# Kernel tuning notes

Measured on AMD Instinct MI355X. Metric: run time of the kernel, lower is better.

## Reference

```python
import jax, jax.numpy as jnp
import numpy as np

B, N, IN_DIM, HID, OUT_DIM, CODEBOOK = 32, 2048, 128, 64, 64, 2048


def setup_inputs() -> dict:
    key = jax.random.key(0)
    ks = jax.random.split(key, 6)
    # xavier-uniform-ish scales for the MLP weights
    def xavier(k, fan_in, fan_out):
        gain = float(np.sqrt(2.0))  # relu gain
        lim = gain * np.sqrt(6.0 / (fan_in + fan_out))
        return jax.random.uniform(k, (fan_in, fan_out), jnp.float32, -lim, lim)
    return {
        "obs": jax.random.normal(ks[0], (B, N, IN_DIM), jnp.float32),
        "W1": xavier(ks[1], IN_DIM, HID),
        "b1": jnp.full((HID,), 0.01, jnp.float32),
        "W2": xavier(ks[2], HID, HID),
        "b2": jnp.full((HID,), 0.01, jnp.float32),
        "W3": xavier(ks[3], HID, OUT_DIM),
        "b3": jnp.full((OUT_DIM,), 0.01, jnp.float32),
        "codebook": jax.random.normal(ks[4], (CODEBOOK, OUT_DIM), jnp.float32),
    }


def reference(obs, W1, b1, W2, b2, W3, b3, codebook):
    # --- tiny MLP ---
    h = jax.nn.relu(obs @ W1 + b1)
    h = jax.nn.relu(h @ W2 + b2)
    x = h @ W3 + b3  # [B, N, D]

    # --- vector quantize: euclidean nearest codebook entry ---
    x2 = jnp.sum(x * x, axis=-1, keepdims=True)           # [B, N, 1]
    e2 = jnp.sum(codebook * codebook, axis=-1)            # [C]
    dist = x2 - 2.0 * jnp.einsum("bnd,cd->bnc", x, codebook) + e2  # [B, N, C]
    idx = jnp.argmin(dist, axis=-1)                        # [B, N] int
    quantize = codebook[idx]                               # [B, N, D] gather

    # commitment loss: mse(sg(quantize), x)
    cmt_loss = jnp.mean((jax.lax.stop_gradient(quantize) - x) ** 2)
    # straight-through estimator
    msg = x + jax.lax.stop_gradient(quantize - x)
    return (msg, idx, cmt_loss)
```

## Files before the change

kernel.cpp:

```cpp
#include <hip/hip_runtime.h>


#define NPTS    65536
#define IN_DIM  128
#define HID     64
#define OUT_DIM 64
#define CB_N    2048
#define MSG_ELEMS (NPTS * OUT_DIM)
#define LOSS_SCALE (1.0f / 4194304.0f)
#define MARG 0.5f
#define CAND_CAP 1024
#define BPTS 128
#define NTHR 512

typedef __attribute__((ext_vector_type(8))) short short8;
typedef _Float16 half8 __attribute__((ext_vector_type(8)));
typedef __attribute__((ext_vector_type(4))) float f32x4;
typedef unsigned int u32;
typedef unsigned long long u64;

__device__ __forceinline__ void gld16(void* lds_base, const void* gsrc) {
    __builtin_amdgcn_global_load_lds(
        (const __attribute__((address_space(1))) u32*)gsrc,
        (__attribute__((address_space(3))) u32*)lds_base, 16, 0, 0);
}

__global__ __launch_bounds__(256) void prep_all(
    const float* __restrict__ cb,
    const float* __restrict__ W1, const float* __restrict__ W2,
    const float* __restrict__ W3,
    float* __restrict__ e2,
    _Float16* __restrict__ cbh,
    _Float16* __restrict__ w1h, _Float16* __restrict__ w1l,
    _Float16* __restrict__ w2h, _Float16* __restrict__ w2l,
    _Float16* __restrict__ w3h, _Float16* __restrict__ w3l,
    float* __restrict__ loss)
{
    const int b = blockIdx.x, tid = threadIdx.x;
    if (b < 64) {
        const int id = b * 256 + tid;
        const int n = id >> 3, h = (id >> 2) & 1, quad = id & 3;
        const int t = n >> 4, l15 = n & 15;
        const float* src = cb + (long)n * OUT_DIM + h * 32 + quad * 8;
        half8 hi;
        #pragma unroll
        for (int j = 0; j < 8; ++j)
            hi[j] = (_Float16)src[j];
        const long dst = ((long)(t * 2 + h) * 64 + quad * 16 + l15) * 8;
        *(half8*)(cbh + dst) = hi;
    } else if (b < 72) {
        const int id = (b - 64) * 256 + tid;
        const int lane = id & 63;
        const int m = lane & 15, quad = lane >> 4;
        const float* W; _Float16 *dh, *dl; int frag;
        if (id < 1024)      { W = W1; dh = w1h; dl = w1l; frag = id >> 6; }
        else if (id < 1536) { W = W2; dh = w2h; dl = w2l; frag = (id - 1024) >> 6; }
        else                { W = W3; dh = w3h; dl = w3l; frag = (id - 1536) >> 6; }
        const int kc = frag >> 2, nt = frag & 3;
        half8 hi, lo;
        #pragma unroll
        for (int j = 0; j < 8; ++j) {
            const float v = W[(long)(kc * 32 + quad * 8 + j) * 64 + nt * 16 + m];
            hi[j] = (_Float16)v;
            lo[j] = (_Float16)(v - (float)hi[j]);
        }
        const long dst = (long)(frag * 64 + lane) * 8;
        *(half8*)(dh + dst) = hi;
        *(half8*)(dl + dst) = lo;
    } else {
        if (b == 72 && tid == 0) *loss = 0.0f;
        const int c = (b - 72) * 256 + tid;
        const float4* row = (const float4*)(cb + (long)c * OUT_DIM);
        float s = 0.0f;
        #pragma unroll
        for (int mq = 0; mq < 16; ++mq) {
            const float4 v = row[mq];
            s += v.x * v.x + v.y * v.y + v.z * v.z + v.w * v.w;
        }
        e2[c] = s;
    }
}

#define MFMA16(A, B, C) __builtin_amdgcn_mfma_f32_16x16x32_f16(A, B, C, 0, 0, 0)

__device__ __forceinline__ void split16(const float* xs, half8& h, half8& l) {
    #pragma unroll
    for (int j = 0; j < 8; ++j) {
        h[j] = (_Float16)xs[j];
        l[j] = (_Float16)(xs[j] - (float)h[j]);
    }
}

__device__ __forceinline__ u64 packkey(float d, int n) {
    u32 ub = __float_as_uint(d);
    ub = (ub & 0x80000000u) ? ~ub : (ub | 0x80000000u);
    return ((u64)ub << 32) | (u32)n;
}

__device__ __forceinline__ float exdist(
    const float* xr, const float* __restrict__ cbrow, float e2v)
{
    const float4* xp = (const float4*)xr;
    const float4* cp = (const float4*)cbrow;
    float a0 = 0.0f, a1 = 0.0f;
    #pragma unroll
    for (int mq = 0; mq < 16; ++mq) {
        const float4 xv = xp[mq], cv = cp[mq];
        a0 = fmaf(xv.x, cv.x, a0); a1 = fmaf(xv.y, cv.y, a1);
        a0 = fmaf(xv.z, cv.z, a0); a1 = fmaf(xv.w, cv.w, a1);
    }
    return fmaf(-2.0f, a0 + a1, e2v);
}

__global__ __launch_bounds__(NTHR, 4) void fused_mlp_vq(
    const float* __restrict__ obs,
    const float* __restrict__ b1, const float* __restrict__ b2,
    const float* __restrict__ b3,
    const _Float16* __restrict__ w1h, const _Float16* __restrict__ w1l,
    const _Float16* __restrict__ w2h, const _Float16* __restrict__ w2l,
    const _Float16* __restrict__ w3h, const _Float16* __restrict__ w3l,
    const float* __restrict__ cb,
    const _Float16* __restrict__ cbhp,
    const float* __restrict__ e2,
    float* __restrict__ msg,
    float* __restrict__ idx_out,
    float* __restrict__ loss_out)
{
    __shared__ float hbuf[BPTS * 68];
    __shared__ __align__(16) char stg[2][16384];
    __shared__ int   cand_pc[CAND_CAP];
    __shared__ u64   keys[BPTS];
    __shared__ int   win_sh[BPTS];
    __shared__ int   idx_sh[BPTS];
    __shared__ float wred[NTHR / 64];
    __shared__ int   cand_cnt;

    const int t = threadIdx.x, lane = t & 63, w = t >> 6;
    const int m = lane & 15, quad = lane >> 4;
    const long base = (long)blockIdx.x * BPTS;
    const int row0 = w * 16 + quad * 4;
    const int arow_l = w * 16 + m;

    if (t == 0) cand_cnt = 0;
    if (t < BPTS) keys[t] = ~0ULL;

    {
        float bb1[4], bb2[4], bb3[4];
        #pragma unroll
        for (int nt = 0; nt < 4; ++nt) {
            bb1[nt] = b1[nt * 16 + m];
            bb2[nt] = b2[nt * 16 + m];
            bb3[nt] = b3[nt * 16 + m];
        }

        const float* arow = obs + (base + w * 16 + m) * IN_DIM;
        half8 a1h[4], a1l[4];
        #pragma unroll
        for (int kc = 0; kc < 4; ++kc) {
            const float4 va = *(const float4*)(arow + kc * 32 + quad * 8);
            const float4 vb = *(const float4*)(arow + kc * 32 + quad * 8 + 4);
            const float xs[8] = {va.x, va.y, va.z, va.w, vb.x, vb.y, vb.z, vb.w};
            split16(xs, a1h[kc], a1l[kc]);
        }

        #pragma unroll
        for (int nt = 0; nt < 4; ++nt) {
            f32x4 acc = {0.0f, 0.0f, 0.0f, 0.0f};
            #pragma unroll
            for (int kc = 0; kc < 4; ++kc) {
                const long fo = (long)((kc * 4 + nt) * 64 + lane) * 8;
                const half8 wh = *(const half8*)(w1h + fo);
                const half8 wl = *(const half8*)(w1l + fo);
                acc = MFMA16(a1h[kc], wh, acc);
                acc = MFMA16(a1l[kc], wh, acc);
                acc = MFMA16(a1h[kc], wl, acc);
            }
            #pragma unroll
            for (int r = 0; r < 4; ++r) {
                const float v = acc[r] + bb1[nt];
                hbuf[(row0 + r) * 68 + nt * 16 + m] = v > 0.0f ? v : 0.0f;
            }
        }

        half8 a2h[2], a2l[2];
        #pragma unroll
        for (int kc = 0; kc < 2; ++kc) {
            const float4 va = *(const float4*)&hbuf[arow_l * 68 + kc * 32 + quad * 8];
            const float4 vb = *(const float4*)&hbuf[arow_l * 68 + kc * 32 + quad * 8 + 4];
            const float xs[8] = {va.x, va.y, va.z, va.w, vb.x, vb.y, vb.z, vb.w};
            split16(xs, a2h[kc], a2l[kc]);
        }
        #pragma unroll
        for (int nt = 0; nt < 4; ++nt) {
            f32x4 acc = {0.0f, 0.0f, 0.0f, 0.0f};
            #pragma unroll
            for (int kc = 0; kc < 2; ++kc) {
                const long fo = (long)((kc * 4 + nt) * 64 + lane) * 8;
                const half8 wh = *(const half8*)(w2h + fo);
                const half8 wl = *(const half8*)(w2l + fo);
                acc = MFMA16(a2h[kc], wh, acc);
                acc = MFMA16(a2l[kc], wh, acc);
                acc = MFMA16(a2h[kc], wl, acc);
            }
            #pragma unroll
            for (int r = 0; r < 4; ++r) {
                const float v = acc[r] + bb2[nt];
                hbuf[(row0 + r) * 68 + nt * 16 + m] = v > 0.0f ? v : 0.0f;
            }
        }

        half8 a3h[2], a3l[2];
        #pragma unroll
        for (int kc = 0; kc < 2; ++kc) {
            const float4 va = *(const float4*)&hbuf[arow_l * 68 + kc * 32 + quad * 8];
            const float4 vb = *(const float4*)&hbuf[arow_l * 68 + kc * 32 + quad * 8 + 4];
            const float xs[8] = {va.x, va.y, va.z, va.w, vb.x, vb.y, vb.z, vb.w};
            split16(xs, a3h[kc], a3l[kc]);
        }
        #pragma unroll
        for (int nt = 0; nt < 4; ++nt) {
            f32x4 acc = {0.0f, 0.0f, 0.0f, 0.0f};
            #pragma unroll
            for (int kc = 0; kc < 2; ++kc) {
                const long fo = (long)((kc * 4 + nt) * 64 + lane) * 8;
                const half8 wh = *(const half8*)(w3h + fo);
                const half8 wl = *(const half8*)(w3l + fo);
                acc = MFMA16(a3h[kc], wh, acc);
                acc = MFMA16(a3l[kc], wh, acc);
                acc = MFMA16(a3h[kc], wl, acc);
            }
            #pragma unroll
            for (int r = 0; r < 4; ++r)
                hbuf[(row0 + r) * 68 + nt * 16 + m] = acc[r] + bb3[nt];
        }
    }

    half8 a0h, a1h;
    {
        const float* xrow = &hbuf[(w * 16 + m) * 68];
        const float4 xa = *(const float4*)(xrow + quad * 8);
        const float4 xb = *(const float4*)(xrow + quad * 8 + 4);
        const float4 xc = *(const float4*)(xrow + 32 + quad * 8);
        const float4 xd = *(const float4*)(xrow + 32 + quad * 8 + 4);
        const float x0[8] = {xa.x, xa.y, xa.z, xa.w, xb.x, xb.y, xb.z, xb.w};
        const float x1[8] = {xc.x, xc.y, xc.z, xc.w, xd.x, xd.y, xd.z, xd.w};
        #pragma unroll
        for (int j = 0; j < 8; ++j) {
            a0h[j] = (_Float16)x0[j];
            a1h[j] = (_Float16)x1[j];
        }
    }

    #pragma unroll
    for (int j = 0; j < 2; ++j)
        gld16(stg[0] + (w * 2 + j) * 1024,
              cbhp + (w * 2 + j) * 512 + lane * 8);
    __syncthreads();

    float bd[4] = {3.4e38f, 3.4e38f, 3.4e38f, 3.4e38f};
    int   bi[4] = {0, 0, 0, 0};

    for (int ph = 0; ph < 16; ++ph) {
        if (ph < 15) {
            const _Float16* cbq = cbhp + (long)(ph + 1) * 8192;
            #pragma unroll
            for (int j = 0; j < 2; ++j)
                gld16(stg[(ph + 1) & 1] + (w * 2 + j) * 1024,
                      cbq + (w * 2 + j) * 512 + lane * 8);
        }
        const char* bufp = stg[ph & 1];

        half8 th[16];
        float e2v[8];
        #pragma unroll
        for (int tl = 0; tl < 8; ++tl) {
            th[tl * 2]     = *(const half8*)(bufp + tl * 2048 + lane * 16);
            th[tl * 2 + 1] = *(const half8*)(bufp + tl * 2048 + 1024 + lane * 16);
            e2v[tl] = e2[(ph * 8 + tl) * 16 + m];
        }

        f32x4 acc[8];
        __builtin_amdgcn_s_setprio(1);
        #pragma unroll
        for (int tl = 0; tl < 8; ++tl) {
            f32x4 z = {0.0f, 0.0f, 0.0f, 0.0f};
            z = MFMA16(a0h, th[tl * 2], z);
            z = MFMA16(a1h, th[tl * 2 + 1], z);
            acc[tl] = z;
        }
        __builtin_amdgcn_s_setprio(0);

        #pragma unroll
        for (int tl = 0; tl < 8; ++tl) {
            const int g = ph * 8 + tl;
            const int code = g * 16 + m;
            bool pushm[4]; int pip[4];
            #pragma unroll
            for (int r = 0; r < 4; ++r) {
                const float d = fmaf(-2.0f, acc[tl][r], e2v[tl]);
                const bool lt = d < bd[r];
                pushm[r] = __builtin_fabsf(d - bd[r]) < MARG;
                pip[r] = lt ? bi[r] : code;
                bd[r] = lt ? d : bd[r];
                bi[r] = lt ? code : bi[r];
            }
            if (__any((int)(pushm[0] | pushm[1] | pushm[2] | pushm[3]))) {
                #pragma unroll
                for (int r = 0; r < 4; ++r) {
                    if (pushm[r]) {
                        const int slot = atomicAdd(&cand_cnt, 1);
                        if (slot < CAND_CAP)
                            cand_pc[slot] = ((w * 16 + quad * 4 + r) << 16) | pip[r];
                    }
                }
            }
        }
        __syncthreads();
    }

    {
        float rd[4]; int ri[4];
        #pragma unroll
        for (int r = 0; r < 4; ++r) { rd[r] = bd[r]; ri[r] = bi[r]; }
        #pragma unroll
        for (int off = 1; off <= 8; off <<= 1) {
            #pragma unroll
            for (int r = 0; r < 4; ++r) {
                const float od = __shfl_xor(rd[r], off, 64);
                const int   oi = __shfl_xor(ri[r], off, 64);
                if (od < rd[r] || (od == rd[r] && oi < ri[r])) {
                    rd[r] = od; ri[r] = oi;
                }
            }
        }
        #pragma unroll
        for (int r = 0; r < 4; ++r) {
            const int pl = w * 16 + quad * 4 + r;
            if (m == 0) win_sh[pl] = ri[r];
            if (bd[r] <= rd[r] + MARG && bi[r] != ri[r]) {
                const int slot = atomicAdd(&cand_cnt, 1);
                if (slot < CAND_CAP)
                    cand_pc[slot] = (pl << 16) | bi[r];
            }
        }
    }
    __syncthreads();

    {
        if (t < BPTS) {
            const int n = win_sh[t];
            const float ex = exdist(&hbuf[t * 68], cb + (long)n * OUT_DIM, e2[n]);
            atomicMin(&keys[t], packkey(ex, n));
        }
        const int L = min(cand_cnt, CAND_CAP);
        for (int l = t; l < L; l += NTHR) {
            const int pc = cand_pc[l];
            const int p = pc >> 16, n = pc & 0xFFFF;
            const float ex = exdist(&hbuf[p * 68], cb + (long)n * OUT_DIM, e2[n]);
            atomicMin(&keys[p], packkey(ex, n));
        }
    }
    __syncthreads();

    if (t < BPTS) {
        const int code = (int)(keys[t] & 0xFFFFFFFFu);
        idx_sh[t] = code;
        idx_out[base + t] = (float)code;
    }
    __syncthreads();

    float lsum = 0.0f;
    float4* mg = (float4*)(msg + base * OUT_DIM);
    #pragma unroll
    for (int mm = 0; mm < 4; ++mm) {
        const int v = t + NTHR * mm;
        const int p = v >> 4, k4 = v & 15;
        const int code = idx_sh[p];
        const float4 q = ((const float4*)(cb + (long)code * OUT_DIM))[k4];
        const float4 xv = *(const float4*)&hbuf[p * 68 + k4 * 4];
        const float dx = q.x - xv.x, dy = q.y - xv.y;
        const float dz = q.z - xv.z, dw2 = q.w - xv.w;
        lsum += dx * dx + dy * dy + dz * dz + dw2 * dw2;
        mg[v] = q;
    }
    #pragma unroll
    for (int off = 32; off > 0; off >>= 1) lsum += __shfl_down(lsum, off, 64);
    if (lane == 0) wred[w] = lsum;
    __syncthreads();
    if (t == 0) {
        float s = 0.0f;
        #pragma unroll
        for (int i = 0; i < NTHR / 64; ++i) s += wred[i];
        atomicAdd(loss_out, s * LOSS_SCALE);
    }
}

extern "C" void kernel_launch(void* const* d_in, const int* in_sizes, int n_in,
                              void* d_out, int out_size, void* d_ws, size_t ws_size,
                              hipStream_t stream) {
    const float* obs = (const float*)d_in[0];
    const float* W1  = (const float*)d_in[1];
    const float* b1  = (const float*)d_in[2];
    const float* W2  = (const float*)d_in[3];
    const float* b2  = (const float*)d_in[4];
    const float* W3  = (const float*)d_in[5];
    const float* b3  = (const float*)d_in[6];
    const float* cb  = (const float*)d_in[7];

    float* out  = (float*)d_out;
    float* msg  = out;
    float* idxf = out + MSG_ELEMS;
    float* loss = out + MSG_ELEMS + NPTS;

    char* ws = (char*)d_ws;
    float*     e2  = (float*)ws;
    _Float16*  cbh = (_Float16*)(ws + 8192);
    _Float16* w1h = (_Float16*)(ws + 532480);
    _Float16* w1l = (_Float16*)(ws + 548864);
    _Float16* w2h = (_Float16*)(ws + 565248);
    _Float16* w2l = (_Float16*)(ws + 573440);
    _Float16* w3h = (_Float16*)(ws + 581632);
    _Float16* w3l = (_Float16*)(ws + 589824);

    prep_all<<<80, 256, 0, stream>>>(cb, W1, W2, W3, e2, cbh,
                                     w1h, w1l, w2h, w2l, w3h, w3l, loss);
    fused_mlp_vq<<<NPTS / BPTS, NTHR, 0, stream>>>(
        obs, b1, b2, b3, w1h, w1l, w2h, w2l, w3h, w3l,
        cb, cbh, e2, msg, idxf, loss);
}
```

Before: 157.0 us.

## Stagger codebook phase order per block and aggregate candidate atomics per wave

Each block now starts its walk over the 16 codebook chunks at an offset derived from its block index, so concurrent blocks read different parts of the codebook instead of the same lines at once. Candidate pushes into the shared list now use one ballot-based atomicAdd per wave with mbcnt prefix offsets, replacing one LDS atomic per pushing lane. The point is to spread L2 traffic and cut contention on the shared counter. It adds some ballot and popcount work on the push path, and the changed visiting order can change tie-breaking in the running argmin.

```diff
diff --git a/kernel.cpp b/kernel.cpp
--- a/kernel.cpp
+++ b/kernel.cpp
@@ -140,6 +140,7 @@
     const long base = (long)blockIdx.x * BPTS;
     const int row0 = w * 16 + quad * 4;
     const int arow_l = w * 16 + m;
+    const int ofs = blockIdx.x & 15;
 
     if (t == 0) cand_cnt = 0;
     if (t < BPTS) keys[t] = ~0ULL;
@@ -254,15 +255,17 @@
     #pragma unroll
     for (int j = 0; j < 2; ++j)
         gld16(stg[0] + (w * 2 + j) * 1024,
-              cbhp + (w * 2 + j) * 512 + lane * 8);
+              cbhp + (long)ofs * 8192 + (w * 2 + j) * 512 + lane * 8);
     __syncthreads();
 
     float bd[4] = {3.4e38f, 3.4e38f, 3.4e38f, 3.4e38f};
     int   bi[4] = {0, 0, 0, 0};
 
     for (int ph = 0; ph < 16; ++ph) {
+        const int pp = (ph + ofs) & 15;
         if (ph < 15) {
-            const _Float16* cbq = cbhp + (long)(ph + 1) * 8192;
+            const int pn = (ph + 1 + ofs) & 15;
+            const _Float16* cbq = cbhp + (long)pn * 8192;
             #pragma unroll
             for (int j = 0; j < 2; ++j)
                 gld16(stg[(ph + 1) & 1] + (w * 2 + j) * 1024,
@@ -276,7 +279,7 @@
         for (int tl = 0; tl < 8; ++tl) {
             th[tl * 2]     = *(const half8*)(bufp + tl * 2048 + lane * 16);
             th[tl * 2 + 1] = *(const half8*)(bufp + tl * 2048 + 1024 + lane * 16);
-            e2v[tl] = e2[(ph * 8 + tl) * 16 + m];
+            e2v[tl] = e2[(pp * 8 + tl) * 16 + m];
         }
 
         f32x4 acc[8];
@@ -292,7 +295,7 @@
 
         #pragma unroll
         for (int tl = 0; tl < 8; ++tl) {
-            const int g = ph * 8 + tl;
+            const int g = pp * 8 + tl;
             const int code = g * 16 + m;
             bool pushm[4]; int pip[4];
             #pragma unroll
@@ -305,13 +308,30 @@
                 bi[r] = lt ? code : bi[r];
             }
             if (__any((int)(pushm[0] | pushm[1] | pushm[2] | pushm[3]))) {
+                u64 mk[4]; int cnt[4];
+                int tot = 0;
+                #pragma unroll
+                for (int r = 0; r < 4; ++r) {
+                    mk[r] = __ballot((int)pushm[r]);
+                    cnt[r] = __popcll(mk[r]);
+                    tot += cnt[r];
+                }
+                int sb = 0;
+                if (lane == 0) sb = atomicAdd(&cand_cnt, tot);
+                sb = __shfl(sb, 0, 64);
+                int pre = 0;
                 #pragma unroll
                 for (int r = 0; r < 4; ++r) {
                     if (pushm[r]) {
-                        const int slot = atomicAdd(&cand_cnt, 1);
+                        const int off = pre + __builtin_amdgcn_mbcnt_hi(
+                            (u32)(mk[r] >> 32),
+                            __builtin_amdgcn_mbcnt_lo((u32)mk[r], 0));
+                        const int slot = sb + off;
                         if (slot < CAND_CAP)
-                            cand_pc[slot] = ((w * 16 + quad * 4 + r) << 16) | pip[r];
+                            cand_pc[slot] =
+                                ((w * 16 + quad * 4 + r) << 16) | pip[r];
                     }
+                    pre += cnt[r];
                 }
             }
         }
```

Measured after the change: 161.8 us. +3.1%, slower.
